# Performance work log

Measured on AMD Instinct MI355X. Metric: run time of the kernel, lower is better.

Reference implementation:

```python
import jax, jax.numpy as jnp
import numpy as np

WS = 8      # window size
NH = 8      # num heads
DIM = 128   # channels


def _rel_index(ws):
    # Swin relative-position index, identical to the torch buffer construction
    coords = np.stack(np.meshgrid(np.arange(ws), np.arange(ws), indexing='ij')).reshape(2, -1)
    rel = (coords[:, :, None] - coords[:, None, :]).transpose(1, 2, 0)  # [N,N,2]
    rel[:, :, 0] += ws - 1
    rel[:, :, 1] += ws - 1
    rel[:, :, 0] *= 2 * ws - 1
    return rel.sum(-1)  # [N,N] in [0, (2ws-1)^2)


def setup_inputs() -> dict:
    key = jax.random.key(0)
    ks = jax.random.split(key, 4)
    return {
        'x': jax.random.normal(ks[0], (2, DIM, 256, 256), jnp.float32),
        'qkv_w': jax.random.normal(ks[1], (3 * DIM, DIM), jnp.float32) * 0.02,
        'qkv_b': jnp.zeros((3 * DIM,), jnp.float32),
        'proj_w': jax.random.normal(ks[2], (DIM, DIM), jnp.float32) * 0.02,
        'proj_b': jnp.zeros((DIM,), jnp.float32),
        'rel_bias': jax.random.normal(ks[3], ((2 * WS - 1) ** 2, NH), jnp.float32) * 0.02,
        'rel_index': jnp.asarray(_rel_index(WS), jnp.int32),
    }


def reference(x, qkv_w, qkv_b, proj_w, proj_b, rel_bias, rel_index):
    B, C, H, W = x.shape
    ws, nh = WS, NH
    hd = C // nh
    scale = hd ** -0.5
    pad_h = (-H) % ws
    pad_w = (-W) % ws
    x = jnp.pad(x, ((0, 0), (0, 0), (0, pad_h), (0, pad_w)))
    Hp, Wp = H + pad_h, W + pad_w
    N = ws * ws
    # window partition -> tokens [B*nWh*nWw, N, C] (channels-last; 1x1 conv == linear)
    xw = x.reshape(B, C, Hp // ws, ws, Wp // ws, ws)
    xw = xw.transpose(0, 2, 4, 3, 5, 1).reshape(-1, N, C)
    qkv = xw @ qkv_w.T + qkv_b                      # [Bw, N, 3C]
    q, k, v = jnp.split(qkv, 3, axis=-1)

    def heads(t):  # [Bw, N, C] -> [Bw, nh, N, hd]
        return t.reshape(t.shape[0], N, nh, hd).transpose(0, 2, 1, 3)

    q, k, v = heads(q), heads(k), heads(v)
    attn = jnp.einsum('bhid,bhjd->bhij', q, k) * scale   # [Bw, nh, N, N]
    bias = rel_bias[rel_index].transpose(2, 0, 1)        # [nh, N, N]
    attn = jax.nn.softmax(attn + bias[None], axis=-1)
    out = jnp.einsum('bhij,bhjd->bhid', attn, v)         # [Bw, nh, N, hd]
    out = out.transpose(0, 2, 1, 3).reshape(-1, N, C)    # [Bw, N, C]
    # window un-partition -> [B, C, Hp, Wp]
    out = out.reshape(B, Hp // ws, Wp // ws, ws, ws, C)
    out = out.transpose(0, 5, 1, 3, 2, 4).reshape(B, C, Hp, Wp)
    out = out[:, :, :H, :W]
    # proj: 1x1 conv
    return jnp.einsum('bchw,oc->bohw', out, proj_w) + proj_b[None, :, None, None]
```

## Files before the change

kernel.cpp:

```cpp
#include <hip/hip_runtime.h>

#define CDIM 128
#define NHEADS 8
#define HD 16
#define NTOK 64
#define HW 65536
#define XSTR 136
#define VSTR 72
#define KST 16
#define SLOT 2304
#define LOG2E 1.44269504088896f

typedef short s8v __attribute__((ext_vector_type(8)));
typedef short s4v __attribute__((ext_vector_type(4)));
typedef float f4v __attribute__((ext_vector_type(4)));

static __device__ __forceinline__ short f2bf(float f) {
    unsigned u = __float_as_uint(f);
    u += 0x7FFFu + ((u >> 16) & 1u);
    return (short)(u >> 16);
}
static __device__ __forceinline__ unsigned cvt2(float lo, float hi) {
    unsigned r;
    asm("v_cvt_pk_bf16_f32 %0, %1, %2" : "=v"(r) : "v"(lo), "v"(hi));
    return r;
}
static __device__ __forceinline__ uint2 pk4(float a, float b, float c, float d) {
    return make_uint2(cvt2(a, b), cvt2(c, d));
}

__global__ __launch_bounds__(256) void pack_w_kernel(
    const float* __restrict__ qkv_w, const float* __restrict__ proj_w,
    short* __restrict__ wpk)
{
    int idx = blockIdx.x * 256 + threadIdx.x;
    int lane = idx & 63, kc = (idx >> 6) & 3, ob = idx >> 8;
    int row = (ob < 24) ? ob * 16 + (lane & 15) : (ob - 24) * 16 + (lane & 15);
    int col = kc * 32 + (lane >> 4) * 8;
    const float* src = ((ob < 24) ? qkv_w : proj_w) + (size_t)row * CDIM + col;
    float sc = (ob < 8) ? 0.25f * LOG2E : 1.0f;
    float4 f0 = *(const float4*)src;
    float4 f1 = *(const float4*)(src + 4);
    s8v r;
    r[0] = f2bf(f0.x * sc); r[1] = f2bf(f0.y * sc);
    r[2] = f2bf(f0.z * sc); r[3] = f2bf(f0.w * sc);
    r[4] = f2bf(f1.x * sc); r[5] = f2bf(f1.y * sc);
    r[6] = f2bf(f1.z * sc); r[7] = f2bf(f1.w * sc);
    *(s8v*)&wpk[(size_t)idx * 8] = r;
}

__global__ __launch_bounds__(256) void pack_b_kernel(
    const float* __restrict__ rel_bias, const int* __restrict__ rel_index,
    float* __restrict__ biasf)
{
    int idx = blockIdx.x * 256 + threadIdx.x;
    int lane = idx & 63, nt = (idx >> 6) & 3, mq = (idx >> 8) & 3, h = idx >> 10;
    int tq  = mq * 16 + (lane & 15);
    int tk0 = nt * 16 + (lane >> 4) * 4;
    f4v v;
    #pragma unroll
    for (int r = 0; r < 4; ++r)
        v[r] = LOG2E * rel_bias[rel_index[tq * 64 + tk0 + r] * NHEADS + h];
    *(f4v*)&biasf[(size_t)idx * 4] = v;
}

__global__ __launch_bounds__(256, 4) void winattn_kernel(
    const float* __restrict__ x, const float* __restrict__ qkv_b,
    const float* __restrict__ proj_b, const short* __restrict__ wpk,
    const float* __restrict__ biasf, float* __restrict__ out)
{
    __shared__ __align__(16) short xs[NTOK * XSTR];
    __shared__ __align__(16) short vsc[4 * SLOT];

    const int tid  = threadIdx.x;
    const int lane = tid & 63;
    const int wv   = tid >> 6;
    const int qd   = lane >> 4;
    const int l15  = lane & 15;
    short* myv = &vsc[wv * SLOT];

    const int wid = (blockIdx.x & 7) * 256 + (blockIdx.x >> 3);
    const int b   = wid >> 10;
    const int wy  = (wid >> 5) & 31, wx = wid & 31;
    const int h0  = wy * 8, w0 = wx * 8;
    const float* xb = x + (size_t)b * CDIM * HW;

    #pragma unroll
    for (int it = 0; it < 8; ++it) {
        const int g   = it * 4 + wv;
        const int cg  = g & 15, tqg = g >> 4;
        const int c   = cg * 8 + ((lane >> 3) & 7);
        const int tq  = tqg * 8 + (lane & 7);
        const int t0  = tq * 4;
        float4 f = *(const float4*)&xb[(size_t)c * HW + (h0 + (t0 >> 3)) * 256 + w0 + (t0 & 7)];
        const int col = ((cg ^ (tq & 7)) << 3) | (c & 7);
        xs[(t0 + 0) * XSTR + col] = f2bf(f.x);
        xs[(t0 + 1) * XSTR + col] = f2bf(f.y);
        xs[(t0 + 2) * XSTR + col] = f2bf(f.z);
        xs[(t0 + 3) * XSTR + col] = f2bf(f.w);
    }
    __syncthreads();

    s8v vf[2][2];
    s8v kf[2][4];
    const int kswz = (l15 >> 1) & 2;
    {
        s8v X[4][4];
        #pragma unroll
        for (int tb = 0; tb < 4; ++tb)
            #pragma unroll
            for (int kc = 0; kc < 4; ++kc) {
                const int gr = ((4 * kc + qd) ^ ((4 * tb + (l15 >> 2)) & 7)) << 3;
                X[tb][kc] = *(const s8v*)&xs[(tb * 16 + l15) * XSTR + gr];
            }

        const s8v* wf = (const s8v*)wpk;

        #pragma unroll
        for (int hp = 0; hp < 2; ++hp) {
            const int h = wv + hp * 4;
            const int ob = 16 + h;
            s8v Wv[4];
            #pragma unroll
            for (int kc = 0; kc < 4; ++kc) Wv[kc] = wf[(ob * 4 + kc) * 64 + lane];
            short* vw = myv + hp * 16 * VSTR;
            const float vb = qkv_b[256 + h * 16 + l15];
            #pragma unroll
            for (int tb = 0; tb < 4; ++tb) {
                f4v acc = {0.f, 0.f, 0.f, 0.f};
                #pragma unroll
                for (int kc = 0; kc < 4; ++kc)
                    acc = __builtin_amdgcn_mfma_f32_16x16x32_bf16(X[tb][kc], Wv[kc], acc, 0, 0, 0);
                *(uint2*)&vw[l15 * VSTR + tb * 16 + qd * 4] =
                    pk4(acc[0] + vb, acc[1] + vb, acc[2] + vb, acc[3] + vb);
            }
            vf[hp][0] = *(const s8v*)&vw[l15 * VSTR + qd * 8];
            vf[hp][1] = *(const s8v*)&vw[l15 * VSTR + 32 + qd * 8];
        }

        #pragma unroll
        for (int hp = 0; hp < 2; ++hp) {
            const int h = wv + hp * 4;
            const int ob = 8 + h;
            s8v Wk[4];
            #pragma unroll
            for (int kc = 0; kc < 4; ++kc) Wk[kc] = wf[(ob * 4 + kc) * 64 + lane];
            float4 kb = *(const float4*)&qkv_b[128 + h * 16 + qd * 4];
            #pragma unroll
            for (int tb = 0; tb < 4; ++tb) {
                f4v acc = {0.f, 0.f, 0.f, 0.f};
                #pragma unroll
                for (int kc = 0; kc < 4; ++kc)
                    acc = __builtin_amdgcn_mfma_f32_16x16x32_bf16(Wk[kc], X[tb][kc], acc, 0, 0, 0);
                *(uint2*)&myv[((hp * 64 + tb * 16 + l15) << 4) + ((qd ^ kswz) << 2)] =
                    pk4(acc[0] + kb.x, acc[1] + kb.y, acc[2] + kb.z, acc[3] + kb.w);
            }
        }

        s8v Wq[2][4];
        #pragma unroll
        for (int hp = 0; hp < 2; ++hp) {
            const int ob = wv + hp * 4;
            #pragma unroll
            for (int kc = 0; kc < 4; ++kc) Wq[hp][kc] = wf[(ob * 4 + kc) * 64 + lane];
        }

        __syncthreads();

        #pragma unroll
        for (int hp = 0; hp < 2; ++hp) {
            const int h = wv + hp * 4;
            float4 qb = *(const float4*)&qkv_b[h * 16 + qd * 4];
            const float qsc = 0.25f * LOG2E;
            #pragma unroll
            for (int tb = 0; tb < 4; ++tb) {
                f4v acc = {0.f, 0.f, 0.f, 0.f};
                #pragma unroll
                for (int kc = 0; kc < 4; ++kc)
                    acc = __builtin_amdgcn_mfma_f32_16x16x32_bf16(Wq[hp][kc], X[tb][kc], acc, 0, 0, 0);
                *(uint2*)&xs[(tb * 16 + l15) * XSTR + h * 16 + qd * 4] =
                    pk4(acc[0] + qb.x * qsc, acc[1] + qb.y * qsc,
                        acc[2] + qb.z * qsc, acc[3] + qb.w * qsc);
            }
        }

        const s8v z8 = {};
        #pragma unroll
        for (int hp = 0; hp < 2; ++hp)
            #pragma unroll
            for (int nt = 0; nt < 4; ++nt) {
                s8v kr = *(const s8v*)&myv[((hp * 64 + nt * 16 + l15) << 4) +
                                           (((2 * (qd & 1)) ^ kswz) << 2)];
                kf[hp][nt] = (qd < 2) ? kr : z8;
            }
    }

    short* os = xs;
    #pragma unroll
    for (int mq = 0; mq < 4; ++mq) {
        f4v bf[2][4];
        #pragma unroll
        for (int hp = 0; hp < 2; ++hp) {
            const int h = wv + hp * 4;
            #pragma unroll
            for (int nt = 0; nt < 4; ++nt)
                bf[hp][nt] = *(const f4v*)&biasf[(size_t)(((h * 4 + mq) * 4 + nt) * 64 + lane) * 4];
        }
        s8v qf[2];
        #pragma unroll
        for (int hp = 0; hp < 2; ++hp) {
            const int h = wv + hp * 4;
            qf[hp] = *(const s8v*)&xs[(mq * 16 + l15) * XSTR + h * 16 + (qd & 1) * 8];
        }
        f4v sv[2][4];
        #pragma unroll
        for (int hp = 0; hp < 2; ++hp)
            #pragma unroll
            for (int nt = 0; nt < 4; ++nt) {
                f4v s = {0.f, 0.f, 0.f, 0.f};
                s = __builtin_amdgcn_mfma_f32_16x16x32_bf16(kf[hp][nt], qf[hp], s, 0, 0, 0);
                sv[hp][nt] = s + bf[hp][nt];
            }
        float mx[2];
        #pragma unroll
        for (int hp = 0; hp < 2; ++hp) {
            f4v a01, a23, a;
            #pragma unroll
            for (int r = 0; r < 4; ++r) {
                a01[r] = fmaxf(sv[hp][0][r], sv[hp][1][r]);
                a23[r] = fmaxf(sv[hp][2][r], sv[hp][3][r]);
            }
            #pragma unroll
            for (int r = 0; r < 4; ++r) a[r] = fmaxf(a01[r], a23[r]);
            float m = fmaxf(fmaxf(a[0], a[1]), fmaxf(a[2], a[3]));
            m = fmaxf(m, __shfl_xor(m, 16, 64));
            m = fmaxf(m, __shfl_xor(m, 32, 64));
            mx[hp] = m;
        }
        float inv[2];
        #pragma unroll
        for (int hp = 0; hp < 2; ++hp) {
            #pragma unroll
            for (int nt = 0; nt < 4; ++nt)
                #pragma unroll
                for (int r = 0; r < 4; ++r)
                    sv[hp][nt][r] = exp2f(sv[hp][nt][r] - mx[hp]);
            f4v s01 = sv[hp][0] + sv[hp][1];
            f4v s23 = sv[hp][2] + sv[hp][3];
            f4v s4  = s01 + s23;
            float sm = (s4[0] + s4[1]) + (s4[2] + s4[3]);
            sm += __shfl_xor(sm, 16, 64);
            sm += __shfl_xor(sm, 32, 64);
            inv[hp] = 1.f / sm;
        }
        #pragma unroll
        for (int hp = 0; hp < 2; ++hp) {
            const int h = wv + hp * 4;
            short* pw = myv + hp * 16 * VSTR;
            #pragma unroll
            for (int nt = 0; nt < 4; ++nt)
                *(uint2*)&pw[l15 * VSTR + nt * 16 + qd * 4] =
                    pk4(sv[hp][nt][0] * inv[hp], sv[hp][nt][1] * inv[hp],
                        sv[hp][nt][2] * inv[hp], sv[hp][nt][3] * inv[hp]);
            s8v pa0 = *(const s8v*)&pw[l15 * VSTR + qd * 8];
            s8v pa1 = *(const s8v*)&pw[l15 * VSTR + 32 + qd * 8];
            f4v O = {0.f, 0.f, 0.f, 0.f};
            O = __builtin_amdgcn_mfma_f32_16x16x32_bf16(pa0, vf[hp][0], O, 0, 0, 0);
            O = __builtin_amdgcn_mfma_f32_16x16x32_bf16(pa1, vf[hp][1], O, 0, 0, 0);
            #pragma unroll
            for (int r = 0; r < 4; ++r)
                os[(mq * 16 + qd * 4 + r) * XSTR + h * HD + l15] = f2bf(O[r]);
        }
    }

    const s8v* wf = (const s8v*)wpk;
    s8v B[2][4];
    float pb2[2]; int o2[2];
    #pragma unroll
    for (int nt = 0; nt < 2; ++nt) {
        const int ob = 24 + wv * 2 + nt;
        o2[nt] = (wv * 2 + nt) * 16 + l15;
        pb2[nt] = proj_b[o2[nt]];
        #pragma unroll
        for (int kc = 0; kc < 4; ++kc) B[nt][kc] = wf[(ob * 4 + kc) * 64 + lane];
    }
    __syncthreads();
    {
        s8v A[4][4];
        #pragma unroll
        for (int mt = 0; mt < 4; ++mt)
            #pragma unroll
            for (int kc = 0; kc < 4; ++kc)
                A[mt][kc] = *(const s8v*)&xs[(mt * 16 + l15) * XSTR + kc * 32 + qd * 8];

        #pragma unroll
        for (int mt = 0; mt < 4; ++mt) {
            const int t0 = mt * 16 + qd * 4;
            const int pix = (h0 + (t0 >> 3)) * 256 + w0 + (t0 & 7);
            #pragma unroll
            for (int nt = 0; nt < 2; ++nt) {
                f4v acc = {0.f, 0.f, 0.f, 0.f};
                #pragma unroll
                for (int kc = 0; kc < 4; ++kc)
                    acc = __builtin_amdgcn_mfma_f32_16x16x32_bf16(A[mt][kc], B[nt][kc], acc, 0, 0, 0);
                float4 v = make_float4(acc[0] + pb2[nt], acc[1] + pb2[nt],
                                       acc[2] + pb2[nt], acc[3] + pb2[nt]);
                *(float4*)&out[((size_t)(b * CDIM + o2[nt])) * HW + pix] = v;
            }
        }
    }
}

extern "C" void kernel_launch(void* const* d_in, const int* in_sizes, int n_in,
                              void* d_out, int out_size, void* d_ws, size_t ws_size,
                              hipStream_t stream) {
    const float* x        = (const float*)d_in[0];
    const float* qkv_w    = (const float*)d_in[1];
    const float* qkv_b    = (const float*)d_in[2];
    const float* proj_w   = (const float*)d_in[3];
    const float* proj_b   = (const float*)d_in[4];
    const float* rel_bias = (const float*)d_in[5];
    const int*   rel_index= (const int*)d_in[6];
    float* out = (float*)d_out;

    short* wpk   = (short*)d_ws;
    float* biasf = (float*)((char*)d_ws + 131072);

    pack_w_kernel<<<32, 256, 0, stream>>>(qkv_w, proj_w, wpk);
    pack_b_kernel<<<32, 256, 0, stream>>>(rel_bias, rel_index, biasf);
    winattn_kernel<<<2048, 256, 0, stream>>>(x, qkv_b, proj_b, wpk, biasf, out);
}
```

Baseline: 181.5 us.

## Process two horizontally adjacent windows per 512-thread block

Each block now handles two neighbouring 8x8 windows side by side, using 8 waves, with each group of four waves owning one window's LDS slice. Loads and stores of x and out now cover 16 contiguous pixels per row across the two windows rather than 8, which should improve coalescing and cache-line use on the strided NCHW layout. Blocks are also mapped linearly instead of with the previous interleaved swizzle. In exchange, LDS per block doubles and the larger blocks coarsen occupancy granularity; __launch_bounds__(512,4) may also tighten the register budget.

```diff
diff --git a/kernel.cpp b/kernel.cpp
--- a/kernel.cpp
+++ b/kernel.cpp
@@ -7,7 +7,6 @@
 #define HW 65536
 #define XSTR 136
 #define VSTR 72
-#define KST 16
 #define SLOT 2304
 #define LOG2E 1.44269504088896f
 
@@ -64,40 +63,44 @@
     *(f4v*)&biasf[(size_t)idx * 4] = v;
 }
 
-__global__ __launch_bounds__(256, 4) void winattn_kernel(
+__global__ __launch_bounds__(512, 4) void winattn_kernel(
     const float* __restrict__ x, const float* __restrict__ qkv_b,
     const float* __restrict__ proj_b, const short* __restrict__ wpk,
     const float* __restrict__ biasf, float* __restrict__ out)
 {
-    __shared__ __align__(16) short xs[NTOK * XSTR];
-    __shared__ __align__(16) short vsc[4 * SLOT];
+    __shared__ __align__(16) short xs[2 * NTOK * XSTR];
+    __shared__ __align__(16) short vsc[8 * SLOT];
 
     const int tid  = threadIdx.x;
     const int lane = tid & 63;
     const int wv   = tid >> 6;
+    const int win  = wv >> 2;
+    const int w4   = wv & 3;
     const int qd   = lane >> 4;
     const int l15  = lane & 15;
-    short* myv = &vsc[wv * SLOT];
-
-    const int wid = (blockIdx.x & 7) * 256 + (blockIdx.x >> 3);
-    const int b   = wid >> 10;
-    const int wy  = (wid >> 5) & 31, wx = wid & 31;
-    const int h0  = wy * 8, w0 = wx * 8;
+    short* myxs = &xs[win * NTOK * XSTR];
+    short* myv  = &vsc[wv * SLOT];
+
+    const int wid = blockIdx.x;
+    const int b   = wid >> 9;
+    const int rem = wid & 511;
+    const int wy  = rem >> 4, kx = rem & 15;
+    const int h0  = wy * 8, w0 = kx * 16 + win * 8;
     const float* xb = x + (size_t)b * CDIM * HW;
 
     #pragma unroll
     for (int it = 0; it < 8; ++it) {
-        const int g   = it * 4 + wv;
+        const int g   = it * 4 + w4;
         const int cg  = g & 15, tqg = g >> 4;
         const int c   = cg * 8 + ((lane >> 3) & 7);
         const int tq  = tqg * 8 + (lane & 7);
         const int t0  = tq * 4;
         float4 f = *(const float4*)&xb[(size_t)c * HW + (h0 + (t0 >> 3)) * 256 + w0 + (t0 & 7)];
         const int col = ((cg ^ (tq & 7)) << 3) | (c & 7);
-        xs[(t0 + 0) * XSTR + col] = f2bf(f.x);
-        xs[(t0 + 1) * XSTR + col] = f2bf(f.y);
-        xs[(t0 + 2) * XSTR + col] = f2bf(f.z);
-        xs[(t0 + 3) * XSTR + col] = f2bf(f.w);
+        myxs[(t0 + 0) * XSTR + col] = f2bf(f.x);
+        myxs[(t0 + 1) * XSTR + col] = f2bf(f.y);
+        myxs[(t0 + 2) * XSTR + col] = f2bf(f.z);
+        myxs[(t0 + 3) * XSTR + col] = f2bf(f.w);
     }
     __syncthreads();
 
@@ -111,14 +114,14 @@
             #pragma unroll
             for (int kc = 0; kc < 4; ++kc) {
                 const int gr = ((4 * kc + qd) ^ ((4 * tb + (l15 >> 2)) & 7)) << 3;
-                X[tb][kc] = *(const s8v*)&xs[(tb * 16 + l15) * XSTR + gr];
+                X[tb][kc] = *(const s8v*)&myxs[(tb * 16 + l15) * XSTR + gr];
             }
 
         const s8v* wf = (const s8v*)wpk;
 
         #pragma unroll
         for (int hp = 0; hp < 2; ++hp) {
-            const int h = wv + hp * 4;
+            const int h = w4 + hp * 4;
             const int ob = 16 + h;
             s8v Wv[4];
             #pragma unroll
@@ -140,7 +143,7 @@
 
         #pragma unroll
         for (int hp = 0; hp < 2; ++hp) {
-            const int h = wv + hp * 4;
+            const int h = w4 + hp * 4;
             const int ob = 8 + h;
             s8v Wk[4];
             #pragma unroll
@@ -160,7 +163,7 @@
         s8v Wq[2][4];
         #pragma unroll
         for (int hp = 0; hp < 2; ++hp) {
-            const int ob = wv + hp * 4;
+            const int ob = w4 + hp * 4;
             #pragma unroll
             for (int kc = 0; kc < 4; ++kc) Wq[hp][kc] = wf[(ob * 4 + kc) * 64 + lane];
         }
@@ -169,7 +172,7 @@
 
         #pragma unroll
         for (int hp = 0; hp < 2; ++hp) {
-            const int h = wv + hp * 4;
+            const int h = w4 + hp * 4;
             float4 qb = *(const float4*)&qkv_b[h * 16 + qd * 4];
             const float qsc = 0.25f * LOG2E;
             #pragma unroll
@@ -178,7 +181,7 @@
                 #pragma unroll
                 for (int kc = 0; kc < 4; ++kc)
                     acc = __builtin_amdgcn_mfma_f32_16x16x32_bf16(Wq[hp][kc], X[tb][kc], acc, 0, 0, 0);
-                *(uint2*)&xs[(tb * 16 + l15) * XSTR + h * 16 + qd * 4] =
+                *(uint2*)&myxs[(tb * 16 + l15) * XSTR + h * 16 + qd * 4] =
                     pk4(acc[0] + qb.x * qsc, acc[1] + qb.y * qsc,
                         acc[2] + qb.z * qsc, acc[3] + qb.w * qsc);
             }
@@ -195,13 +198,13 @@
             }
     }
 
-    short* os = xs;
+    short* os = myxs;
     #pragma unroll
     for (int mq = 0; mq < 4; ++mq) {
         f4v bf[2][4];
         #pragma unroll
         for (int hp = 0; hp < 2; ++hp) {
-            const int h = wv + hp * 4;
+            const int h = w4 + hp * 4;
             #pragma unroll
             for (int nt = 0; nt < 4; ++nt)
                 bf[hp][nt] = *(const f4v*)&biasf[(size_t)(((h * 4 + mq) * 4 + nt) * 64 + lane) * 4];
@@ -209,8 +212,8 @@
         s8v qf[2];
         #pragma unroll
         for (int hp = 0; hp < 2; ++hp) {
-            const int h = wv + hp * 4;
-            qf[hp] = *(const s8v*)&xs[(mq * 16 + l15) * XSTR + h * 16 + (qd & 1) * 8];
+            const int h = w4 + hp * 4;
+            qf[hp] = *(const s8v*)&myxs[(mq * 16 + l15) * XSTR + h * 16 + (qd & 1) * 8];
         }
         f4v sv[2][4];
         #pragma unroll
@@ -255,7 +258,7 @@
         }
         #pragma unroll
         for (int hp = 0; hp < 2; ++hp) {
-            const int h = wv + hp * 4;
+            const int h = w4 + hp * 4;
             short* pw = myv + hp * 16 * VSTR;
             #pragma unroll
             for (int nt = 0; nt < 4; ++nt)
@@ -278,8 +281,8 @@
     float pb2[2]; int o2[2];
     #pragma unroll
     for (int nt = 0; nt < 2; ++nt) {
-        const int ob = 24 + wv * 2 + nt;
-        o2[nt] = (wv * 2 + nt) * 16 + l15;
+        const int ob = 24 + w4 * 2 + nt;
+        o2[nt] = (w4 * 2 + nt) * 16 + l15;
         pb2[nt] = proj_b[o2[nt]];
         #pragma unroll
         for (int kc = 0; kc < 4; ++kc) B[nt][kc] = wf[(ob * 4 + kc) * 64 + lane];
@@ -291,7 +294,7 @@
         for (int mt = 0; mt < 4; ++mt)
             #pragma unroll
             for (int kc = 0; kc < 4; ++kc)
-                A[mt][kc] = *(const s8v*)&xs[(mt * 16 + l15) * XSTR + kc * 32 + qd * 8];
+                A[mt][kc] = *(const s8v*)&myxs[(mt * 16 + l15) * XSTR + kc * 32 + qd * 8];
 
         #pragma unroll
         for (int mt = 0; mt < 4; ++mt) {
@@ -328,5 +331,5 @@
 
     pack_w_kernel<<<32, 256, 0, stream>>>(qkv_w, proj_w, wpk);
     pack_b_kernel<<<32, 256, 0, stream>>>(rel_bias, rel_index, biasf);
-    winattn_kernel<<<2048, 256, 0, stream>>>(x, qkv_b, proj_b, wpk, biasf, out);
-}
+    winattn_kernel<<<1024, 512, 0, stream>>>(x, qkv_b, proj_b, wpk, biasf, out);
+}
```

Result: slower. 189.2 us (+4.2%).
